# Kernel optimization log

Hardware: AMD Instinct MI355X
Metric: run time of the kernel (lower is better)

Reference implementation:

```python
import jax, jax.numpy as jnp
import numpy as np

D_MODEL = 1024
NHEAD = 16
D_FF = 4096
LN_EPS = 1e-5


def _layer_norm(x, g, b):
    mu = jnp.mean(x, axis=-1, keepdims=True)
    var = jnp.mean(jnp.square(x - mu), axis=-1, keepdims=True)
    return (x - mu) * jax.lax.rsqrt(var + LN_EPS) * g + b


def setup_inputs() -> dict:
    key = jax.random.key(0)
    ks = jax.random.split(key, 12)
    d, f = D_MODEL, D_FF
    s = 1.0 / np.sqrt(d)
    inp = {
        "src": jax.random.normal(ks[0], (2, 2048, d), dtype=jnp.float32),
        "Wq": jax.random.uniform(ks[1], (d, d), jnp.float32, -s, s),
        "bq": jnp.zeros((d,), jnp.float32),
        "Wk": jax.random.uniform(ks[2], (d, d), jnp.float32, -s, s),
        "bk": jnp.zeros((d,), jnp.float32),
        "Wv": jax.random.uniform(ks[3], (d, d), jnp.float32, -s, s),
        "bv": jnp.zeros((d,), jnp.float32),
        "Wo": jax.random.uniform(ks[4], (d, d), jnp.float32, -s, s),
        "bo": jnp.zeros((d,), jnp.float32),
        "W1": jax.random.uniform(ks[5], (d, f), jnp.float32, -s, s),
        "b1": jnp.zeros((f,), jnp.float32),
        "W2": jax.random.uniform(ks[6], (f, d), jnp.float32, -1.0 / np.sqrt(f), 1.0 / np.sqrt(f)),
        "b2": jnp.zeros((d,), jnp.float32),
        "ln1_g": jnp.ones((d,), jnp.float32),
        "ln1_b": jnp.zeros((d,), jnp.float32),
        "ln2_g": jnp.ones((d,), jnp.float32),
        "ln2_b": jnp.zeros((d,), jnp.float32),
    }
    return inp


def reference(src, Wq, bq, Wk, bk, Wv, bv, Wo, bo, W1, b1, W2, b2,
              ln1_g, ln1_b, ln2_g, ln2_b):
    B, S, D = src.shape
    H = NHEAD
    hd = D // H
    # QKV projections, split into heads: [B, H, S, hd]
    q = (src @ Wq + bq).reshape(B, S, H, hd).transpose(0, 2, 1, 3)
    k = (src @ Wk + bk).reshape(B, S, H, hd).transpose(0, 2, 1, 3)
    v = (src @ Wv + bv).reshape(B, S, H, hd).transpose(0, 2, 1, 3)
    # Explicit full-score attention (no mask branch), as in source.
    scores = jnp.einsum("bhqd,bhkd->bhqk", q, k) / jnp.sqrt(jnp.asarray(hd, src.dtype))
    attn = jax.nn.softmax(scores, axis=-1)
    ctx = jnp.einsum("bhqk,bhkd->bhqd", attn, v)
    ctx = ctx.transpose(0, 2, 1, 3).reshape(B, S, D)
    src2 = ctx @ Wo + bo
    x = _layer_norm(src + src2, ln1_g, ln1_b)
    ff = jax.nn.relu(x @ W1 + b1) @ W2 + b2
    out = _layer_norm(x + ff, ln2_g, ln2_b)
    return out
```

## Files before the change

kernel.cpp:

```cpp
#include <hip/hip_runtime.h>
#include <cstdint>
#include <cstddef>

#define SEQ 2048
#define BATCH 2
#define ROWS (BATCH * SEQ)

typedef __attribute__((ext_vector_type(8))) short short8;
typedef __attribute__((ext_vector_type(4))) float f32x4;
typedef __attribute__((ext_vector_type(16))) float f32x16;
typedef __attribute__((ext_vector_type(8))) _Float16 half8;
typedef __attribute__((ext_vector_type(2))) __fp16 fp16x2;

__device__ __forceinline__ unsigned short f2bf(float f) {
  union { float f; uint32_t u; } v; v.f = f;
  uint32_t r = v.u + 0x7fffu + ((v.u >> 16) & 1u);
  return (unsigned short)(r >> 16);
}

__device__ __forceinline__ unsigned short bf2h(unsigned short b) {
  union { uint32_t u; float f; } v; v.u = ((uint32_t)b) << 16;
  union { _Float16 h; unsigned short u; } o; o.h = (_Float16)v.f;
  return o.u;
}

__device__ __forceinline__ void async16(const void* g, void* l) {
  __builtin_amdgcn_global_load_lds((const __attribute__((address_space(1))) void*)g,
                                   (__attribute__((address_space(3))) void*)l, 16, 0, 0);
}

__global__ __launch_bounds__(256) void prep_kernel(
    const float* __restrict__ src,
    const float* __restrict__ Wq, const float* __restrict__ Wk,
    const float* __restrict__ Wv, const float* __restrict__ Wo,
    const float* __restrict__ W1, const float* __restrict__ W2,
    const float* __restrict__ bq, const float* __restrict__ bk,
    const float* __restrict__ bv,
    unsigned short* __restrict__ qkvT, unsigned short* __restrict__ WoT,
    unsigned short* __restrict__ W1T, unsigned short* __restrict__ W2T,
    float* __restrict__ biasq, unsigned short* __restrict__ xbf) {
  const int blk = blockIdx.x;
  if (blk < 12288) {
    const float* W; unsigned short* WT; int K, N, nbx, base; float scale = 1.0f;
    if (blk < 1024)      { W = Wq; WT = qkvT;             K = 1024; N = 1024; nbx = 32;  base = 0;    scale = 0.18033688f; }
    else if (blk < 2048) { W = Wk; WT = qkvT + 1048576;   K = 1024; N = 1024; nbx = 32;  base = 1024; }
    else if (blk < 3072) { W = Wv; WT = qkvT + 2097152;   K = 1024; N = 1024; nbx = 32;  base = 2048; }
    else if (blk < 4096) { W = Wo; WT = WoT;              K = 1024; N = 1024; nbx = 32;  base = 3072; }
    else if (blk < 8192) { W = W1; WT = W1T;              K = 1024; N = 4096; nbx = 128; base = 4096; }
    else                 { W = W2; WT = W2T;              K = 4096; N = 1024; nbx = 32;  base = 8192; }
    const int lb = blk - base;
    const int bx = lb % nbx, by = lb / nbx;
    __shared__ float t[32][33];
    const int tx = threadIdx.x & 31, ty = threadIdx.x >> 5;
    const int n0 = bx * 32, k0 = by * 32;
    for (int i = ty; i < 32; i += 8)
      t[i][tx] = W[(size_t)(k0 + i) * N + n0 + tx];
    __syncthreads();
    for (int i = ty; i < 32; i += 8)
      WT[(size_t)(n0 + i) * K + k0 + tx] = f2bf(t[tx][i] * scale);
  } else if (blk < 12300) {
    int i = (blk - 12288) * 256 + threadIdx.x;
    float v = (i < 1024) ? bq[i] * 0.18033688f : (i < 2048 ? bk[i - 1024] : bv[i - 2048]);
    biasq[i] = v;
  } else {
    size_t i = ((size_t)(blk - 12300) * 256 + threadIdx.x) * 4;
    float4 vv = *(const float4*)(src + i);
    ushort4 o;
    o.x = f2bf(vv.x); o.y = f2bf(vv.y); o.z = f2bf(vv.z); o.w = f2bf(vv.w);
    *(ushort4*)(xbf + i) = o;
  }
}

__global__ __launch_bounds__(256) void vtrans(const unsigned short* __restrict__ qkv,
                                              unsigned short* __restrict__ VT) {
  const int st = blockIdx.x, bh = blockIdx.y, b = bh >> 4, h = bh & 15;
  __shared__ unsigned short t[64][72];
  const int tid = threadIdx.x;
#pragma unroll
  for (int it = 0; it < 2; ++it) {
    int i = it * 256 + tid;
    int s = i >> 3, c = (i & 7) * 8;
    short8 v = *(const short8*)(qkv + ((size_t)b * SEQ + st * 64 + s) * 3072 + 2048 + h * 64 + c);
#pragma unroll
    for (int j = 0; j < 8; ++j) t[c + j][s] = bf2h((unsigned short)v[j]);
  }
  __syncthreads();
#pragma unroll
  for (int it = 0; it < 2; ++it) {
    int i = it * 256 + tid;
    int d = i >> 3, sc = (i & 7) * 8;
    short8 o;
#pragma unroll
    for (int j = 0; j < 8; ++j) o[j] = (short)t[d][sc + j];
    *(short8*)(VT + ((size_t)bh * 64 + d) * 2048 + st * 64 + sc) = o;
  }
}

template <bool RELU>
__global__ __launch_bounds__(512, 2) void gemm_8p(
    const unsigned short* __restrict__ A, const unsigned short* __restrict__ BT,
    const float* __restrict__ bias, unsigned short* __restrict__ outB,
    int M, int N, int K) {
  __shared__ __align__(16) unsigned short lds[65536];
  const int tid = threadIdx.x;
  const int lane = tid & 63, ln = lane & 15, quad = lane >> 4;
  const int wid = tid >> 6, wm = wid >> 2, wn = wid & 3;
  const int m0 = blockIdx.y * 256, n0 = blockIdx.x * 256;
  const int srow = tid >> 2, scol = (tid & 3) * 8;
  const unsigned short* Ag0 = A + (size_t)(m0 + srow) * K + scol;
  const unsigned short* Ag1 = A + (size_t)(m0 + srow + 128) * K + scol;
  const unsigned short* Bg0 = BT + (size_t)(n0 + srow) * K + scol;
  const unsigned short* Bg1 = BT + (size_t)(n0 + srow + 128) * K + scol;
  const int sdst = tid * 8;
  f32x4 acc[8][4] = {};
  short8 fa[2][4];
  short8 fb[2][4];
  const int NT = K >> 6;
#pragma unroll
  for (int kh = 0; kh < 2; ++kh) {
    async16(Ag0 + kh * 32, &lds[kh * 8192 + sdst]);
    async16(Ag1 + kh * 32, &lds[kh * 8192 + sdst + 4096]);
    async16(Bg0 + kh * 32, &lds[16384 + kh * 8192 + sdst]);
    async16(Bg1 + kh * 32, &lds[16384 + kh * 8192 + sdst + 4096]);
  }
  asm volatile("s_waitcnt vmcnt(0)" ::: "memory");
  __builtin_amdgcn_s_barrier();
  {
    const unsigned short* ab = &lds[0];
#pragma unroll
    for (int fi = 0; fi < 4; ++fi)
      fa[1][fi] = *(const short8*)&ab[(wm * 128 + fi * 16 + ln) * 32 + quad * 8];
#pragma unroll
    for (int ni = 0; ni < 4; ++ni)
      fb[0][ni] = *(const short8*)&ab[16384 + (wn * 64 + ni * 16 + ln) * 32 + quad * 8];
  }
  for (int t = 0; t < NT; ++t) {
    const int cb = (t & 1) * 32768, nb = cb ^ 32768;
    const bool more = (t + 1 < NT);
    const int knext = (t + 1) * 64;
#pragma unroll
    for (int p = 0; p < 4; ++p) {
      if (p < 3) {
        const int kk2 = (p + 1) >> 1, mh2 = (p + 1) & 1;
        const unsigned short* ab = &lds[cb + kk2 * 8192];
#pragma unroll
        for (int fi = 0; fi < 4; ++fi)
          fa[p & 1][fi] =
              *(const short8*)&ab[(wm * 128 + mh2 * 64 + fi * 16 + ln) * 32 + quad * 8];
        if (p == 1) {
#pragma unroll
          for (int ni = 0; ni < 4; ++ni)
            fb[1][ni] = *(const short8*)&ab[16384 + (wn * 64 + ni * 16 + ln) * 32 + quad * 8];
        }
      } else if (more) {
        const unsigned short* ab = &lds[nb];
#pragma unroll
        for (int fi = 0; fi < 4; ++fi)
          fa[1][fi] = *(const short8*)&ab[(wm * 128 + fi * 16 + ln) * 32 + quad * 8];
#pragma unroll
        for (int ni = 0; ni < 4; ++ni)
          fb[0][ni] = *(const short8*)&ab[16384 + (wn * 64 + ni * 16 + ln) * 32 + quad * 8];
      }
      if (more && p < 2) {
        unsigned short* d = &lds[nb + p * 8192];
        async16(Ag0 + knext + p * 32, d + sdst);
        async16(Ag1 + knext + p * 32, d + sdst + 4096);
        async16(Bg0 + knext + p * 32, d + 16384 + sdst);
        async16(Bg1 + knext + p * 32, d + 16384 + sdst + 4096);
      }
      if (p == 0) {
        if (more) asm volatile("s_waitcnt vmcnt(4)" ::: "memory");
        else      asm volatile("s_waitcnt vmcnt(0)" ::: "memory");
      } else if (p == 2 && more) {
        asm volatile("s_waitcnt vmcnt(4)" ::: "memory");
      }
      __builtin_amdgcn_s_barrier();
      __builtin_amdgcn_s_setprio(1);
#pragma unroll
      for (int fi = 0; fi < 4; ++fi)
#pragma unroll
        for (int ni = 0; ni < 4; ++ni)
          acc[(p & 1) * 4 + fi][ni] = __builtin_amdgcn_mfma_f32_16x16x32_bf16(
              fa[(p + 1) & 1][fi], fb[p >> 1][ni], acc[(p & 1) * 4 + fi][ni], 0, 0, 0);
      __builtin_amdgcn_s_setprio(0);
      if (p < 3 || more) __builtin_amdgcn_s_barrier();
    }
  }
#pragma unroll
  for (int mi = 0; mi < 8; ++mi)
#pragma unroll
    for (int ni = 0; ni < 4; ++ni)
#pragma unroll
      for (int reg = 0; reg < 4; ++reg) {
        int row = m0 + wm * 128 + mi * 16 + quad * 4 + reg;
        int col = n0 + wn * 64 + ni * 16 + ln;
        float v = acc[mi][ni][reg] + bias[col];
        if (RELU) v = fmaxf(v, 0.f);
        outB[(size_t)row * N + col] = f2bf(v);
      }
}

template <bool RELU, bool OUTBF, bool HASRES>
__global__ __launch_bounds__(256) void gemm_bt64(
    const unsigned short* __restrict__ A, const unsigned short* __restrict__ BT,
    const float* __restrict__ bias, const float* __restrict__ Rres,
    float* __restrict__ outF, unsigned short* __restrict__ outB,
    int M, int N, int K) {
  __shared__ unsigned short As[4][128 * 32];
  __shared__ unsigned short Bs[4][64 * 32];
  const int tid = threadIdx.x;
  const int lane = tid & 63, ln = lane & 15, quad = lane >> 4;
  const int w = tid >> 6;
  const int m0 = blockIdx.y * 128, n0 = blockIdx.x * 64;
  const int mw = w * 32;
  f32x4 acc[2][4] = {};
  const int i0 = tid, i1 = tid + 256;
  const int r0 = i0 >> 2, kc0 = (i0 & 3) * 8;
  const int r1 = i1 >> 2, kc1 = (i1 & 3) * 8;
  for (int k0 = 0; k0 < K; k0 += 128) {
    __syncthreads();
#pragma unroll
    for (int p = 0; p < 4; ++p) {
      const int kp = k0 + p * 32;
      async16(A + (size_t)(m0 + r0) * K + kp + kc0, &As[p][i0 * 8]);
      async16(A + (size_t)(m0 + r1) * K + kp + kc1, &As[p][i1 * 8]);
      async16(BT + (size_t)(n0 + r0) * K + kp + kc0, &Bs[p][i0 * 8]);
    }
    __syncthreads();
#pragma unroll
    for (int p = 0; p < 4; ++p) {
      short8 a[2], b[4];
#pragma unroll
      for (int mi = 0; mi < 2; ++mi)
        a[mi] = *(const short8*)&As[p][(mw + mi * 16 + ln) * 32 + quad * 8];
#pragma unroll
      for (int ni = 0; ni < 4; ++ni)
        b[ni] = *(const short8*)&Bs[p][(ni * 16 + ln) * 32 + quad * 8];
#pragma unroll
      for (int mi = 0; mi < 2; ++mi)
#pragma unroll
        for (int ni = 0; ni < 4; ++ni)
          acc[mi][ni] = __builtin_amdgcn_mfma_f32_16x16x32_bf16(a[mi], b[ni], acc[mi][ni], 0, 0, 0);
    }
  }
#pragma unroll
  for (int mi = 0; mi < 2; ++mi) {
#pragma unroll
    for (int ni = 0; ni < 4; ++ni) {
#pragma unroll
      for (int reg = 0; reg < 4; ++reg) {
        int row = m0 + mw + mi * 16 + quad * 4 + reg;
        int col = n0 + ni * 16 + ln;
        float v = acc[mi][ni][reg] + bias[col];
        if (HASRES) v += Rres[(size_t)row * N + col];
        if (RELU) v = fmaxf(v, 0.f);
        if (OUTBF) outB[(size_t)row * N + col] = f2bf(v);
        else outF[(size_t)row * N + col] = v;
      }
    }
  }
}

__global__ __launch_bounds__(128, 2) void attn_kernel(const unsigned short* __restrict__ qkv,
                                                      const unsigned short* __restrict__ VT,
                                                      unsigned short* __restrict__ ctx) {
  const int qt = blockIdx.x;
  const int bh = blockIdx.y, b = bh >> 4, h = bh & 15;
  const int tid = threadIdx.x;
  const int w = tid >> 6, lane = tid & 63;
  const int r32 = lane & 31, hi = lane >> 5, r7 = r32 & 7;
  const int sw2 = (r32 >> 3) & 3;
  __shared__ __align__(16) unsigned short Ks[2 * 4096];
  __shared__ __align__(16) unsigned short Vs[2 * 4096];
  const size_t rowbase = (size_t)b * SEQ;
  const unsigned short* kbase = qkv + rowbase * 3072 + 1024 + h * 64;
  const unsigned short* vbase = VT + (size_t)bh * 64 * 2048;
  int r_[4], s_[4], wsw_[4];
#pragma unroll
  for (int i = 0; i < 4; ++i) {
    int idx = i * 128 + tid;
    r_[i] = idx >> 3; s_[i] = idx & 7;
    wsw_[i] = r_[i] * 64 + ((s_[i] ^ (r_[i] & 7) ^ ((r_[i] >> 3) & 3)) * 8);
  }
  short8 qf[4];
  {
    const unsigned short* qp = qkv + (rowbase + qt * 64 + w * 32 + r32) * 3072 + h * 64;
#pragma unroll
    for (int dc = 0; dc < 4; ++dc) qf[dc] = *(const short8*)(qp + dc * 16 + hi * 8);
  }
  short8 kst[4], vst[4];
#pragma unroll
  for (int i = 0; i < 4; ++i) {
    kst[i] = *(const short8*)(kbase + (size_t)r_[i] * 3072 + s_[i] * 8);
    vst[i] = *(const short8*)(vbase + (size_t)r_[i] * 2048 + s_[i] * 8);
  }
#pragma unroll
  for (int i = 0; i < 4; ++i) {
    *(short8*)&Ks[wsw_[i]] = kst[i];
    *(short8*)&Vs[wsw_[i]] = vst[i];
  }
  __syncthreads();
  f32x16 oacc0 = {}, oacc1 = {};
  float lsum = 0.f;
  int cur = 0;
  for (int kt = 0; kt < 32; ++kt) {
    if (kt < 31) {
      const unsigned short* kp = kbase + (size_t)(kt + 1) * 64 * 3072;
      const unsigned short* vp = vbase + (kt + 1) * 64;
#pragma unroll
      for (int i = 0; i < 4; ++i) {
        kst[i] = *(const short8*)(kp + (size_t)r_[i] * 3072 + s_[i] * 8);
        vst[i] = *(const short8*)(vp + (size_t)r_[i] * 2048 + s_[i] * 8);
      }
    }
    const unsigned short* Kb = &Ks[cur];
    const unsigned short* Vb = &Vs[cur];
    f32x16 z0 = {}, z1 = {};
    __builtin_amdgcn_s_setprio(1);
#pragma unroll
    for (int dc = 0; dc < 4; ++dc) {
      const int sl = (((dc * 2 + hi) ^ r7 ^ sw2) & 7) * 8;
      short8 kf0 = *(const short8*)&Kb[r32 * 64 + sl];
      short8 kf1 = *(const short8*)&Kb[(32 + r32) * 64 + sl];
      z0 = __builtin_amdgcn_mfma_f32_32x32x16_bf16(kf0, qf[dc], z0, 0, 0, 0);
      z1 = __builtin_amdgcn_mfma_f32_32x32x16_bf16(kf1, qf[dc], z1, 0, 0, 0);
    }
    __builtin_amdgcn_s_setprio(0);
    half8 pf[4];
#pragma unroll
    for (int kc = 0; kc < 4; ++kc) {
      float e[8];
#pragma unroll
      for (int j = 0; j < 8; ++j) {
        float zz = (kc < 2) ? z0[(kc & 1) * 8 + j] : z1[(kc & 1) * 8 + j];
        e[j] = __builtin_amdgcn_exp2f(zz);
        lsum += e[j];
      }
      union { fp16x2 hh; unsigned int u; } a0, a1, b0, b1;
      a0.hh = __builtin_amdgcn_cvt_pkrtz(e[0], e[1]);
      a1.hh = __builtin_amdgcn_cvt_pkrtz(e[2], e[3]);
      b0.hh = __builtin_amdgcn_cvt_pkrtz(e[4], e[5]);
      b1.hh = __builtin_amdgcn_cvt_pkrtz(e[6], e[7]);
      asm volatile("v_permlane32_swap_b32 %0, %1" : "+v"(a0.u), "+v"(b0.u));
      asm volatile("v_permlane32_swap_b32 %0, %1" : "+v"(a1.u), "+v"(b1.u));
      union { unsigned int u[4]; half8 hh; } fr;
      fr.u[0] = a0.u; fr.u[1] = a1.u; fr.u[2] = b0.u; fr.u[3] = b1.u;
      pf[kc] = fr.hh;
    }
    __builtin_amdgcn_s_setprio(1);
#pragma unroll
    for (int kc = 0; kc < 4; ++kc) {
      const int sl = (((kc * 2 + hi) ^ r7 ^ sw2) & 7) * 8;
      half8 vf0 = *(const half8*)&Vb[r32 * 64 + sl];
      half8 vf1 = *(const half8*)&Vb[(32 + r32) * 64 + sl];
      oacc0 = __builtin_amdgcn_mfma_f32_32x32x16_f16(vf0, pf[kc], oacc0, 0, 0, 0);
      oacc1 = __builtin_amdgcn_mfma_f32_32x32x16_f16(vf1, pf[kc], oacc1, 0, 0, 0);
    }
    __builtin_amdgcn_s_setprio(0);
    if (kt < 31) {
      const int nb = cur ^ 4096;
#pragma unroll
      for (int i = 0; i < 4; ++i) {
        *(short8*)&Ks[nb + wsw_[i]] = kst[i];
        *(short8*)&Vs[nb + wsw_[i]] = vst[i];
      }
      __syncthreads();
      cur = nb;
    }
  }
  float tot = lsum + __shfl_xor(lsum, 32);
  float rl = 1.0f / tot;
  const size_t orow = (rowbase + (size_t)qt * 64 + w * 32 + r32) * 1024 + h * 64 + hi * 4;
#pragma unroll
  for (int tq = 0; tq < 4; ++tq) {
    ushort4 o0, o1;
    o0.x = f2bf(oacc0[tq * 4 + 0] * rl); o0.y = f2bf(oacc0[tq * 4 + 1] * rl);
    o0.z = f2bf(oacc0[tq * 4 + 2] * rl); o0.w = f2bf(oacc0[tq * 4 + 3] * rl);
    *(ushort4*)(ctx + orow + tq * 8) = o0;
    o1.x = f2bf(oacc1[tq * 4 + 0] * rl); o1.y = f2bf(oacc1[tq * 4 + 1] * rl);
    o1.z = f2bf(oacc1[tq * 4 + 2] * rl); o1.w = f2bf(oacc1[tq * 4 + 3] * rl);
    *(ushort4*)(ctx + orow + 32 + tq * 8) = o1;
  }
}

__global__ __launch_bounds__(256) void ln_kernel(const float* __restrict__ y,
                                                 const float* __restrict__ g,
                                                 const float* __restrict__ bb,
                                                 float* __restrict__ outF,
                                                 unsigned short* __restrict__ outB) {
  const int row = blockIdx.x;
  const int tid = threadIdx.x;
  const float* yr = y + (size_t)row * 1024;
  float v[4]; float s = 0.f, s2 = 0.f;
#pragma unroll
  for (int j = 0; j < 4; ++j) {
    v[j] = yr[tid + j * 256];
    s += v[j]; s2 += v[j] * v[j];
  }
#pragma unroll
  for (int off = 1; off < 64; off <<= 1) {
    s += __shfl_xor(s, off);
    s2 += __shfl_xor(s2, off);
  }
  __shared__ float ws1[4], ws2[4];
  if ((tid & 63) == 0) { ws1[tid >> 6] = s; ws2[tid >> 6] = s2; }
  __syncthreads();
  s = ws1[0] + ws1[1] + ws1[2] + ws1[3];
  s2 = ws2[0] + ws2[1] + ws2[2] + ws2[3];
  const float mu = s * (1.f / 1024.f);
  const float var = s2 * (1.f / 1024.f) - mu * mu;
  const float rstd = rsqrtf(var + 1e-5f);
#pragma unroll
  for (int j = 0; j < 4; ++j) {
    int c = tid + j * 256;
    float val = (v[j] - mu) * rstd * g[c] + bb[c];
    if (outF) outF[(size_t)row * 1024 + c] = val;
    if (outB) outB[(size_t)row * 1024 + c] = f2bf(val);
  }
}

extern "C" void kernel_launch(void* const* d_in, const int* in_sizes, int n_in,
                              void* d_out, int out_size, void* d_ws, size_t ws_size,
                              hipStream_t stream) {
  const float* src = (const float*)d_in[0];
  const float* Wq = (const float*)d_in[1];
  const float* bq = (const float*)d_in[2];
  const float* Wk = (const float*)d_in[3];
  const float* bk = (const float*)d_in[4];
  const float* Wv = (const float*)d_in[5];
  const float* bv = (const float*)d_in[6];
  const float* Wo = (const float*)d_in[7];
  const float* bo = (const float*)d_in[8];
  const float* W1 = (const float*)d_in[9];
  const float* b1 = (const float*)d_in[10];
  const float* W2 = (const float*)d_in[11];
  const float* b2 = (const float*)d_in[12];
  const float* ln1g = (const float*)d_in[13];
  const float* ln1b = (const float*)d_in[14];
  const float* ln2g = (const float*)d_in[15];
  const float* ln2b = (const float*)d_in[16];
  float* out = (float*)d_out;

  char* ws = (char*)d_ws;
  unsigned short* qkvT = (unsigned short*)(ws + 0);
  unsigned short* WoT  = (unsigned short*)(ws + 6291456);
  unsigned short* W1T  = (unsigned short*)(ws + 8388608);
  unsigned short* W2T  = (unsigned short*)(ws + 16777216);
  float*          biasq = (float*)(ws + 25165824);
  unsigned short* xbf  = (unsigned short*)(ws + 25178112);
  unsigned short* qkv  = (unsigned short*)(ws + 33566720);
  unsigned short* hbuf = qkv;
  unsigned short* ctx  = (unsigned short*)(ws + 58732544);
  float*          ybuf = (float*)(ws + 67121152);
  unsigned short* VT   = (unsigned short*)(ws + 67121152);
  float*          xf   = (float*)(ws + 83898368);

  prep_kernel<<<16396, 256, 0, stream>>>(src, Wq, Wk, Wv, Wo, W1, W2, bq, bk, bv,
                                         qkvT, WoT, W1T, W2T, biasq, xbf);

  gemm_8p<false><<<dim3(12, 16), 512, 0, stream>>>(xbf, qkvT, biasq, qkv, ROWS, 3072, 1024);
  vtrans<<<dim3(32, 32), 256, 0, stream>>>(qkv, VT);
  attn_kernel<<<dim3(32, 32), 128, 0, stream>>>(qkv, VT, ctx);
  gemm_bt64<false, false, true><<<dim3(16, 32), 256, 0, stream>>>(
      ctx, WoT, bo, src, ybuf, nullptr, ROWS, 1024, 1024);
  ln_kernel<<<4096, 256, 0, stream>>>(ybuf, ln1g, ln1b, xf, xbf);
  gemm_8p<true><<<dim3(16, 16), 512, 0, stream>>>(xbf, W1T, b1, hbuf, ROWS, 4096, 1024);
  gemm_bt64<false, false, true><<<dim3(16, 32), 256, 0, stream>>>(
      hbuf, W2T, b2, xf, ybuf, nullptr, ROWS, 1024, 4096);
  ln_kernel<<<4096, 256, 0, stream>>>(ybuf, ln2g, ln2b, out, nullptr);
}
```

Baseline: 365.9 us.

## Retile QKV GEMM to 256x192 tiles and swizzle block order in bt64 GEMM

The 8-wave GEMM is templated on the N-tile width so the QKV projection uses 256x192 tiles, launching 256 workgroups instead of 192. This spreads the work more evenly across the GPU's compute units. The B-tile load path and the LDS layout are generalized to match, with the second B half loaded by only 256 threads when NI=3. The 128x64 GEMM also remaps block IDs with an 8-way interleave, meant to change how blocks land across XCDs and improve L2 reuse. The trade-off is a smaller N tile per block, which lowers per-block arithmetic intensity and raises redundant A reads.

```diff
diff --git a/kernel.cpp b/kernel.cpp
--- a/kernel.cpp
+++ b/kernel.cpp
@@ -96,77 +96,87 @@
   }
 }
 
-template <bool RELU>
+template <bool RELU, int NI>
 __global__ __launch_bounds__(512, 2) void gemm_8p(
     const unsigned short* __restrict__ A, const unsigned short* __restrict__ BT,
     const float* __restrict__ bias, unsigned short* __restrict__ outB,
     int M, int N, int K) {
-  __shared__ __align__(16) unsigned short lds[65536];
+  constexpr int BHALF = NI * 2048;
+  constexpr int BUFS = 16384 + NI * 4096;
+  __shared__ __align__(16) unsigned short lds[2 * BUFS];
   const int tid = threadIdx.x;
   const int lane = tid & 63, ln = lane & 15, quad = lane >> 4;
   const int wid = tid >> 6, wm = wid >> 2, wn = wid & 3;
-  const int m0 = blockIdx.y * 256, n0 = blockIdx.x * 256;
+  const int m0 = blockIdx.y * 256, n0 = blockIdx.x * (NI * 64);
   const int srow = tid >> 2, scol = (tid & 3) * 8;
   const unsigned short* Ag0 = A + (size_t)(m0 + srow) * K + scol;
   const unsigned short* Ag1 = A + (size_t)(m0 + srow + 128) * K + scol;
   const unsigned short* Bg0 = BT + (size_t)(n0 + srow) * K + scol;
-  const unsigned short* Bg1 = BT + (size_t)(n0 + srow + 128) * K + scol;
+  const int t2 = (NI == 4) ? tid : (tid & 255);
+  const unsigned short* Bg1 = BT + (size_t)(n0 + 128 + (t2 >> 2)) * K + (t2 & 3) * 8;
   const int sdst = tid * 8;
-  f32x4 acc[8][4] = {};
+  const int bdst2 = 4096 + t2 * 8;
+  f32x4 acc[8][NI] = {};
   short8 fa[2][4];
-  short8 fb[2][4];
+  short8 fb[2][NI];
   const int NT = K >> 6;
 #pragma unroll
   for (int kh = 0; kh < 2; ++kh) {
-    async16(Ag0 + kh * 32, &lds[kh * 8192 + sdst]);
-    async16(Ag1 + kh * 32, &lds[kh * 8192 + sdst + 4096]);
-    async16(Bg0 + kh * 32, &lds[16384 + kh * 8192 + sdst]);
-    async16(Bg1 + kh * 32, &lds[16384 + kh * 8192 + sdst + 4096]);
+    unsigned short* Ad = &lds[kh * 8192];
+    unsigned short* Bd = &lds[16384 + kh * BHALF];
+    async16(Ag0 + kh * 32, Ad + sdst);
+    async16(Ag1 + kh * 32, Ad + sdst + 4096);
+    async16(Bg0 + kh * 32, Bd + sdst);
+    async16(Bg1 + kh * 32, Bd + bdst2);
   }
   asm volatile("s_waitcnt vmcnt(0)" ::: "memory");
   __builtin_amdgcn_s_barrier();
   {
-    const unsigned short* ab = &lds[0];
+    const unsigned short* Ah = &lds[0];
+    const unsigned short* Bh = &lds[16384];
 #pragma unroll
     for (int fi = 0; fi < 4; ++fi)
-      fa[1][fi] = *(const short8*)&ab[(wm * 128 + fi * 16 + ln) * 32 + quad * 8];
-#pragma unroll
-    for (int ni = 0; ni < 4; ++ni)
-      fb[0][ni] = *(const short8*)&ab[16384 + (wn * 64 + ni * 16 + ln) * 32 + quad * 8];
+      fa[1][fi] = *(const short8*)&Ah[(wm * 128 + fi * 16 + ln) * 32 + quad * 8];
+#pragma unroll
+    for (int ni = 0; ni < NI; ++ni)
+      fb[0][ni] = *(const short8*)&Bh[(wn * (NI * 16) + ni * 16 + ln) * 32 + quad * 8];
   }
   for (int t = 0; t < NT; ++t) {
-    const int cb = (t & 1) * 32768, nb = cb ^ 32768;
+    const int cb = (t & 1) * BUFS, nb = cb ^ BUFS;
     const bool more = (t + 1 < NT);
     const int knext = (t + 1) * 64;
 #pragma unroll
     for (int p = 0; p < 4; ++p) {
       if (p < 3) {
         const int kk2 = (p + 1) >> 1, mh2 = (p + 1) & 1;
-        const unsigned short* ab = &lds[cb + kk2 * 8192];
+        const unsigned short* Ah = &lds[cb + kk2 * 8192];
 #pragma unroll
         for (int fi = 0; fi < 4; ++fi)
           fa[p & 1][fi] =
-              *(const short8*)&ab[(wm * 128 + mh2 * 64 + fi * 16 + ln) * 32 + quad * 8];
+              *(const short8*)&Ah[(wm * 128 + mh2 * 64 + fi * 16 + ln) * 32 + quad * 8];
         if (p == 1) {
-#pragma unroll
-          for (int ni = 0; ni < 4; ++ni)
-            fb[1][ni] = *(const short8*)&ab[16384 + (wn * 64 + ni * 16 + ln) * 32 + quad * 8];
+          const unsigned short* Bh = &lds[cb + 16384 + BHALF];
+#pragma unroll
+          for (int ni = 0; ni < NI; ++ni)
+            fb[1][ni] = *(const short8*)&Bh[(wn * (NI * 16) + ni * 16 + ln) * 32 + quad * 8];
         }
       } else if (more) {
-        const unsigned short* ab = &lds[nb];
+        const unsigned short* Ah = &lds[nb];
+        const unsigned short* Bh = &lds[nb + 16384];
 #pragma unroll
         for (int fi = 0; fi < 4; ++fi)
-          fa[1][fi] = *(const short8*)&ab[(wm * 128 + fi * 16 + ln) * 32 + quad * 8];
-#pragma unroll
-        for (int ni = 0; ni < 4; ++ni)
-          fb[0][ni] = *(const short8*)&ab[16384 + (wn * 64 + ni * 16 + ln) * 32 + quad * 8];
+          fa[1][fi] = *(const short8*)&Ah[(wm * 128 + fi * 16 + ln) * 32 + quad * 8];
+#pragma unroll
+        for (int ni = 0; ni < NI; ++ni)
+          fb[0][ni] = *(const short8*)&Bh[(wn * (NI * 16) + ni * 16 + ln) * 32 + quad * 8];
       }
       if (more && p < 2) {
-        unsigned short* d = &lds[nb + p * 8192];
-        async16(Ag0 + knext + p * 32, d + sdst);
-        async16(Ag1 + knext + p * 32, d + sdst + 4096);
-        async16(Bg0 + knext + p * 32, d + 16384 + sdst);
-        async16(Bg1 + knext + p * 32, d + 16384 + sdst + 4096);
+        unsigned short* Ad = &lds[nb + p * 8192];
+        unsigned short* Bd = &lds[nb + 16384 + p * BHALF];
+        async16(Ag0 + knext + p * 32, Ad + sdst);
+        async16(Ag1 + knext + p * 32, Ad + sdst + 4096);
+        async16(Bg0 + knext + p * 32, Bd + sdst);
+        async16(Bg1 + knext + p * 32, Bd + bdst2);
       }
       if (p == 0) {
         if (more) asm volatile("s_waitcnt vmcnt(4)" ::: "memory");
@@ -179,7 +189,7 @@
 #pragma unroll
       for (int fi = 0; fi < 4; ++fi)
 #pragma unroll
-        for (int ni = 0; ni < 4; ++ni)
+        for (int ni = 0; ni < NI; ++ni)
           acc[(p & 1) * 4 + fi][ni] = __builtin_amdgcn_mfma_f32_16x16x32_bf16(
               fa[(p + 1) & 1][fi], fb[p >> 1][ni], acc[(p & 1) * 4 + fi][ni], 0, 0, 0);
       __builtin_amdgcn_s_setprio(0);
@@ -189,11 +199,11 @@
 #pragma unroll
   for (int mi = 0; mi < 8; ++mi)
 #pragma unroll
-    for (int ni = 0; ni < 4; ++ni)
+    for (int ni = 0; ni < NI; ++ni)
 #pragma unroll
       for (int reg = 0; reg < 4; ++reg) {
         int row = m0 + wm * 128 + mi * 16 + quad * 4 + reg;
-        int col = n0 + wn * 64 + ni * 16 + ln;
+        int col = n0 + wn * (NI * 16) + ni * 16 + ln;
         float v = acc[mi][ni][reg] + bias[col];
         if (RELU) v = fmaxf(v, 0.f);
         outB[(size_t)row * N + col] = f2bf(v);
@@ -211,7 +221,10 @@
   const int tid = threadIdx.x;
   const int lane = tid & 63, ln = lane & 15, quad = lane >> 4;
   const int w = tid >> 6;
-  const int m0 = blockIdx.y * 128, n0 = blockIdx.x * 64;
+  const int nwg = gridDim.x * gridDim.y;
+  int bid = blockIdx.y * gridDim.x + blockIdx.x;
+  bid = (bid & 7) * (nwg >> 3) + (bid >> 3);
+  const int m0 = (bid / gridDim.x) * 128, n0 = (bid % gridDim.x) * 64;
   const int mw = w * 32;
   f32x4 acc[2][4] = {};
   const int i0 = tid, i1 = tid + 256;
@@ -458,13 +471,13 @@
   prep_kernel<<<16396, 256, 0, stream>>>(src, Wq, Wk, Wv, Wo, W1, W2, bq, bk, bv,
                                          qkvT, WoT, W1T, W2T, biasq, xbf);
 
-  gemm_8p<false><<<dim3(12, 16), 512, 0, stream>>>(xbf, qkvT, biasq, qkv, ROWS, 3072, 1024);
+  gemm_8p<false, 3><<<dim3(16, 16), 512, 0, stream>>>(xbf, qkvT, biasq, qkv, ROWS, 3072, 1024);
   vtrans<<<dim3(32, 32), 256, 0, stream>>>(qkv, VT);
   attn_kernel<<<dim3(32, 32), 128, 0, stream>>>(qkv, VT, ctx);
   gemm_bt64<false, false, true><<<dim3(16, 32), 256, 0, stream>>>(
       ctx, WoT, bo, src, ybuf, nullptr, ROWS, 1024, 1024);
   ln_kernel<<<4096, 256, 0, stream>>>(ybuf, ln1g, ln1b, xf, xbf);
-  gemm_8p<true><<<dim3(16, 16), 512, 0, stream>>>(xbf, W1T, b1, hbuf, ROWS, 4096, 1024);
+  gemm_8p<true, 4><<<dim3(16, 16), 512, 0, stream>>>(xbf, W1T, b1, hbuf, ROWS, 4096, 1024);
   gemm_bt64<false, false, true><<<dim3(16, 32), 256, 0, stream>>>(
       hbuf, W2T, b2, xf, ybuf, nullptr, ROWS, 1024, 4096);
   ln_kernel<<<4096, 256, 0, stream>>>(ybuf, ln2g, ln2b, out, nullptr);
```

After: 365.3 us. No clear change (-0.2%).
